# Kernel optimization log

Measured on AMD Instinct MI355X. Metric: run time of the kernel, lower is better.

## Reference

```python
import jax, jax.numpy as jnp
import numpy as np


def _conv1x1(x, w, b):
    # x: [B, Cin, T, H, W], w: [Cout, Cin], b: [Cout] -> [B, Cout, T, H, W]
    return jnp.einsum('bcthw,oc->bothw', x, w) + b[None, :, None, None, None]


def setup_inputs() -> dict:
    key = jax.random.key(0)
    ks = jax.random.split(key, 9)
    B, Ci, T, H, W = 2, 128, 4, 32, 32
    Co = 64
    s_in = 1.0 / np.sqrt(Ci)
    s_out = 1.0 / np.sqrt(Co)
    return {
        'z': jax.random.normal(ks[0], (B, Ci, T, H, W), dtype=jnp.float32),
        'w_theta': jax.random.uniform(ks[1], (Co, Ci), jnp.float32, -s_in, s_in),
        'b_theta': jax.random.uniform(ks[2], (Co,), jnp.float32, -s_in, s_in),
        'w_phi': jax.random.uniform(ks[3], (Co, Ci), jnp.float32, -s_in, s_in),
        'b_phi': jax.random.uniform(ks[4], (Co,), jnp.float32, -s_in, s_in),
        'w_psi': jax.random.uniform(ks[5], (Co, Ci), jnp.float32, -s_in, s_in),
        'b_psi': jax.random.uniform(ks[6], (Co,), jnp.float32, -s_in, s_in),
        'w_v': jax.random.uniform(ks[7], (Ci, Co), jnp.float32, -s_out, s_out),
        'b_v': jax.random.uniform(ks[8], (Ci,), jnp.float32, -s_out, s_out),
    }


def reference(z, w_theta, b_theta, w_phi, b_phi, w_psi, b_psi, w_v, b_v):
    B, Ci, T, H, W = z.shape
    Co = w_theta.shape[0]
    N = T * H * W
    # 1x1 conv projections, flattened to [B, Co, N]
    theta = _conv1x1(z, w_theta, b_theta).reshape(B, Co, N)
    phi = _conv1x1(z, w_phi, b_phi).reshape(B, Co, N)
    psi = _conv1x1(z, w_psi, b_psi).reshape(B, Co, N)
    # g = phi^T @ psi : [B, N, N]; normalize with ReLU(g / N)
    g = jnp.einsum('bcn,bcm->bnm', phi, psi)
    norm_g = jax.nn.relu(g / jnp.asarray(N, z.dtype))
    # tmp = norm_g @ theta^T -> [B, N, Co] -> [B, Co, T, H, W]
    tmp = jnp.einsum('bnm,bcm->bcn', norm_g, theta).reshape(B, Co, T, H, W)
    vg = _conv1x1(tmp, w_v, b_v)
    return vg + z
```

## Files before the change

kernel.cpp:

```cpp
#include <hip/hip_runtime.h>


#define NSEQ 4096
#define CI 128
#define CO 64

typedef __attribute__((ext_vector_type(8))) short bf16x8;
typedef __attribute__((ext_vector_type(4))) short bf16x4;
typedef __attribute__((ext_vector_type(4))) float f32x4;
typedef __attribute__((ext_vector_type(16))) float f32x16;

static __device__ inline short f2bf(float f) {
  union { float f; unsigned u; } v; v.f = f;
  unsigned r = v.u + 0x7fffu + ((v.u >> 16) & 1u);
  return (short)(r >> 16);
}
static __device__ inline float bf2f(short s) {
  union { unsigned u; float f; } v; v.u = ((unsigned)(unsigned short)s) << 16;
  return v.f;
}

#define MFMA1632(a, b, c) __builtin_amdgcn_mfma_f32_16x16x32_bf16(a, b, c, 0, 0, 0)
#define MFMA3216(a, b, c) __builtin_amdgcn_mfma_f32_32x32x16_bf16(a, b, c, 0, 0, 0)

#if __has_builtin(__builtin_amdgcn_mfma_f32_16x16x16bf16_1k)
static __device__ inline f32x4 mfma16(bf16x4 a, bf16x4 b, f32x4 c) {
  return __builtin_amdgcn_mfma_f32_16x16x16bf16_1k(a, b, c, 0, 0, 0);
}
#else
static __device__ inline f32x4 mfma16(bf16x4 a, bf16x4 b, f32x4 c) {
  asm("v_mfma_f32_16x16x16_bf16 %0, %1, %2, %0" : "+v"(c) : "v"(a), "v"(b));
  return c;
}
#endif

static __device__ inline unsigned cvt_pk_bf16(float lo, float hi) {
  unsigned d;
  asm("v_cvt_pk_bf16_f32 %0, %1, %2" : "=v"(d) : "v"(lo), "v"(hi));
  return d;
}
static __device__ inline void pl32swap(unsigned& a, unsigned& b) {
  asm("v_permlane32_swap_b32 %0, %1" : "+v"(a), "+v"(b));
}

__global__ __launch_bounds__(256, 2) void proj_kernel(
    const float* __restrict__ z,
    const float* __restrict__ w_th, const float* __restrict__ b_th,
    const float* __restrict__ w_ph, const float* __restrict__ b_ph,
    const float* __restrict__ w_ps, const float* __restrict__ b_ps,
    short* __restrict__ Qg, short* __restrict__ Kg, short* __restrict__ Vt)
{
  const int bid = blockIdx.x;
  const int b = bid >> 8;
  const int n0 = (bid & 255) * 16;
  const int t = threadIdx.x;
  const int w = t >> 6, l = t & 63, lr = l & 15, lg = l >> 4;
  const f32x4 zero4 = {0.f, 0.f, 0.f, 0.f};

  bf16x8 zf[4];
#pragma unroll
  for (int ks = 0; ks < 4; ++ks) {
    const float* zp = z + (size_t)(b * CI + ks * 32 + lg * 8) * NSEQ + n0 + lr;
    float tmp[8];
#pragma unroll
    for (int j = 0; j < 8; ++j) tmp[j] = zp[(size_t)j * NSEQ];
#pragma unroll
    for (int j = 0; j < 8; ++j) zf[ks][j] = f2bf(tmp[j]);
  }

  {
    const float* Wm[2] = {w_ph, w_ps};
    const float* Bm[2] = {b_ph, b_ps};
    short*       Dm[2] = {Qg, Kg};
#pragma unroll
    for (int mt = 0; mt < 2; ++mt) {
      const float sc = (mt == 0) ? (1.0f / 4096.0f) : 1.0f;
      f32x4 acc = zero4;
#pragma unroll
      for (int ks = 0; ks < 4; ++ks) {
        const float* wp = Wm[mt] + (size_t)(w * 16 + lr) * CI + ks * 32 + lg * 8;
        f32x4 x0 = *(const f32x4*)wp;
        f32x4 x1 = *(const f32x4*)(wp + 4);
        bf16x8 wf;
#pragma unroll
        for (int j = 0; j < 4; ++j) { wf[j] = f2bf(x0[j] * sc); wf[4 + j] = f2bf(x1[j] * sc); }
        acc = MFMA1632(wf, zf[ks], acc);
      }
      const f32x4 bias4 = *(const f32x4*)(Bm[mt] + w * 16 + lg * 4);
      bf16x4 pk;
#pragma unroll
      for (int r = 0; r < 4; ++r) pk[r] = f2bf(acc[r] + bias4[r] * sc);
      *(bf16x4*)(Dm[mt] + (size_t)(b * NSEQ + n0 + lr) * CO + w * 16 + lg * 4) = pk;
    }
  }

  {
    f32x4 acc = zero4;
#pragma unroll
    for (int ks = 0; ks < 4; ++ks) {
      const float* wp = w_th + (size_t)(w * 16 + lr) * CI + ks * 32 + lg * 8;
      f32x4 x0 = *(const f32x4*)wp;
      f32x4 x1 = *(const f32x4*)(wp + 4);
      bf16x8 wtf;
#pragma unroll
      for (int j = 0; j < 4; ++j) { wtf[j] = f2bf(x0[j]); wtf[4 + j] = f2bf(x1[j]); }
      acc = MFMA1632(zf[ks], wtf, acc);
    }
    const float bias = b_th[w * 16 + lr];
    bf16x4 pk;
#pragma unroll
    for (int r = 0; r < 4; ++r) pk[r] = f2bf(acc[r] + bias);
    *(bf16x4*)(Vt + (size_t)(b * CO + w * 16 + lr) * NSEQ + n0 + lg * 4) = pk;
  }
}

__global__ __launch_bounds__(256, 4) void attn_kernel(
    const short* __restrict__ Qg, const short* __restrict__ Kg,
    const short* __restrict__ Vt, short* __restrict__ Opart)
{
  __shared__ float red[2][2048];

  const int bid = blockIdx.x;
  const int ms = bid & 7;
  const int u = bid >> 3;
  const int b = u & 1;
  const int nt = u >> 1;
  const int n0 = nt * 32;
  const int t = threadIdx.x;
  const int w = t >> 6, l = t & 63, lc = l & 31, h = l >> 5;
  const int mw = ms * 512 + w * 128;

  bf16x8 qf[4];
  {
    const short* qb = Qg + (size_t)(b * NSEQ + n0 + lc) * CO + h * 8;
#pragma unroll
    for (int ks = 0; ks < 4; ++ks) qf[ks] = *(const bf16x8*)(qb + ks * 16);
  }

  f32x16 oacc[2];
#pragma unroll
  for (int i = 0; i < 2; ++i)
#pragma unroll
    for (int e = 0; e < 16; ++e) oacc[i][e] = 0.f;

#pragma unroll
  for (int it = 0; it < 4; ++it) {
    const int m0 = mw + it * 32;

    bf16x8 kf[4];
    {
      const short* kb = Kg + (size_t)(b * NSEQ + m0 + lc) * CO + h * 8;
#pragma unroll
      for (int ks = 0; ks < 4; ++ks) kf[ks] = *(const bf16x8*)(kb + ks * 16);
    }

    f32x16 s;
#pragma unroll
    for (int e = 0; e < 16; ++e) s[e] = 0.f;
#pragma unroll
    for (int ks = 0; ks < 4; ++ks) s = MFMA3216(kf[ks], qf[ks], s);

    unsigned pk[8];
#pragma unroll
    for (int q = 0; q < 8; ++q)
      pk[q] = cvt_pk_bf16(fmaxf(s[2 * q], 0.f), fmaxf(s[2 * q + 1], 0.f));

    const short* vb = Vt + (size_t)(b * CO + lc) * NSEQ + m0 + h * 8;
#pragma unroll
    for (int kw = 0; kw < 2; ++kw) {
      unsigned x0 = pk[4 * kw + 0], y0 = pk[4 * kw + 2];
      unsigned x1 = pk[4 * kw + 1], y1 = pk[4 * kw + 3];
      pl32swap(x0, y0); pl32swap(x1, y1);
      union { unsigned u[4]; bf16x8 v; } pb = {{x0, x1, y0, y1}};
      bf16x8 vf0 = *(const bf16x8*)(vb + kw * 16);
      bf16x8 vf1 = *(const bf16x8*)(vb + (size_t)32 * NSEQ + kw * 16);
      oacc[0] = MFMA3216(vf0, pb.v, oacc[0]);
      oacc[1] = MFMA3216(vf1, pb.v, oacc[1]);
    }
  }

  if (!(w & 1)) {
#pragma unroll
    for (int osub = 0; osub < 2; ++osub)
#pragma unroll
      for (int rb = 0; rb < 4; ++rb) {
        f32x4 v;
#pragma unroll
        for (int r = 0; r < 4; ++r) v[r] = oacc[osub][rb * 4 + r];
        const int o = osub * 32 + rb * 8 + h * 4;
        const int os = o ^ ((lc & 15) << 2);
        *(f32x4*)&red[w >> 1][lc * 64 + os] = v;
      }
  }
  __syncthreads();
  if (w & 1) {
#pragma unroll
    for (int osub = 0; osub < 2; ++osub)
#pragma unroll
      for (int rb = 0; rb < 4; ++rb) {
        const int o = osub * 32 + rb * 8 + h * 4;
        const int os = o ^ ((lc & 15) << 2);
        float* p = &red[w >> 1][lc * 64 + os];
        f32x4 v = *(f32x4*)p;
#pragma unroll
        for (int r = 0; r < 4; ++r) v[r] += oacc[osub][rb * 4 + r];
        *(f32x4*)p = v;
      }
  }
  __syncthreads();

  short* gout = Opart + (size_t)((b * 128 + nt) * 8 + ms) * 2048;
#pragma unroll
  for (int pass = 0; pass < 2; ++pass) {
    const int lin = pass * 1024 + t * 4;
    const int n = lin >> 6, os4 = lin & 63;
    f32x4 v0 = *(f32x4*)&red[0][lin];
    f32x4 v1 = *(f32x4*)&red[1][lin];
    const int o = os4 ^ ((n & 15) << 2);
    bf16x4 pkv;
#pragma unroll
    for (int r = 0; r < 4; ++r) pkv[r] = f2bf(v0[r] + v1[r]);
    *(bf16x4*)(gout + n * 64 + o) = pkv;
  }
}

__global__ __launch_bounds__(256, 2) void epi_kernel(
    const short* __restrict__ Opart, const float* __restrict__ w_v,
    const float* __restrict__ b_v, const float* __restrict__ z,
    float* __restrict__ out)
{
  __shared__ float Olds[16 * 68];

  const int bid = blockIdx.x;
  const int b = bid >> 8;
  const int n16 = bid & 255;
  const int nt = n16 >> 1, sub = n16 & 1;
  const int n0 = n16 * 16;
  const int t = threadIdx.x;

  {
    const short* src = Opart + (size_t)((b * 128 + nt) * 8) * 2048 + sub * 1024;
    const int n = t >> 4, o4 = (t & 15) * 4;
    f32x4 acc = {0.f, 0.f, 0.f, 0.f};
#pragma unroll
    for (int p = 0; p < 8; ++p) {
      bf16x4 vv = *(const bf16x4*)(src + (size_t)p * 2048 + n * 64 + o4);
#pragma unroll
      for (int j = 0; j < 4; ++j) acc[j] += bf2f(vv[j]);
    }
    *(f32x4*)&Olds[n * 68 + o4] = acc;
  }
  __syncthreads();

  const int w = t >> 6, l = t & 63, lr = l & 15, lg = l >> 4;
  const f32x4 zero4 = {0.f, 0.f, 0.f, 0.f};

  bf16x4 of[4];
#pragma unroll
  for (int osub = 0; osub < 4; ++osub)
#pragma unroll
    for (int j = 0; j < 4; ++j)
      of[osub][j] = f2bf(Olds[lr * 68 + osub * 16 + lg * 4 + j]);

#pragma unroll
  for (int c2 = 0; c2 < 2; ++c2) {
    const int cis = w * 2 + c2;
    bf16x4 wfr[4];
#pragma unroll
    for (int osub = 0; osub < 4; ++osub) {
      f32x4 wl = *(const f32x4*)(w_v + (size_t)(cis * 16 + lr) * CO + osub * 16 + lg * 4);
#pragma unroll
      for (int j = 0; j < 4; ++j) wfr[osub][j] = f2bf(wl[j]);
    }
    const f32x4 bv4 = *(const f32x4*)(b_v + cis * 16 + lg * 4);
    f32x4 e = zero4;
#pragma unroll
    for (int osub = 0; osub < 4; ++osub)
      e = mfma16(wfr[osub], of[osub], e);
#pragma unroll
    for (int r = 0; r < 4; ++r) {
      const int ci = cis * 16 + lg * 4 + r;
      const size_t off = (size_t)(b * CI + ci) * NSEQ + n0 + lr;
      out[off] = e[r] + z[off] + bv4[r];
    }
  }
}

extern "C" void kernel_launch(void* const* d_in, const int* in_sizes, int n_in,
                              void* d_out, int out_size, void* d_ws, size_t ws_size,
                              hipStream_t stream) {
  const float* z    = (const float*)d_in[0];
  const float* w_th = (const float*)d_in[1];
  const float* b_th = (const float*)d_in[2];
  const float* w_ph = (const float*)d_in[3];
  const float* b_ph = (const float*)d_in[4];
  const float* w_ps = (const float*)d_in[5];
  const float* b_ps = (const float*)d_in[6];
  const float* w_v  = (const float*)d_in[7];
  const float* b_v  = (const float*)d_in[8];
  float* out = (float*)d_out;

  short* Qg = (short*)d_ws;
  short* Kg = Qg + 2 * NSEQ * CO;
  short* Vt = Kg + 2 * NSEQ * CO;
  short* Opart = Vt + 2 * NSEQ * CO;

  proj_kernel<<<512, 256, 0, stream>>>(z, w_th, b_th, w_ph, b_ph, w_ps, b_ps,
                                       Qg, Kg, Vt);
  attn_kernel<<<2048, 256, 0, stream>>>(Qg, Kg, Vt, Opart);
  epi_kernel<<<512, 256, 0, stream>>>(Opart, w_v, b_v, z, out);
}
```

Measured before the change: 121.3 us.

## Repartition attention blocks so each wave owns distinct query rows, drop intra-block reduction

Each attention block previously handled 32 query rows, with its 4 waves splitting the key range; the partial outputs were then reduced through LDS across waves. Now each wave owns its own 32 query rows within a 128-row tile and scans 256 keys, and the grid is halved to 1024 blocks with a 16-way key split. The cross-wave LDS reduction and a sync go away, and partials are written transposed as [o][n] with 16-byte stores. In exchange the epilogue must sum 16 partials instead of 8, so Opart traffic roughly doubles, and the key loop is no longer unrolled.

After: 129.2 us. 1.06x slower.

```diff
diff --git a/kernel.cpp b/kernel.cpp
--- a/kernel.cpp
+++ b/kernel.cpp
@@ -118,21 +118,19 @@
     const short* __restrict__ Qg, const short* __restrict__ Kg,
     const short* __restrict__ Vt, short* __restrict__ Opart)
 {
-  __shared__ float red[2][2048];
+  __shared__ float lds_t[64 * 128];
 
   const int bid = blockIdx.x;
-  const int ms = bid & 7;
-  const int u = bid >> 3;
-  const int b = u & 1;
-  const int nt = u >> 1;
-  const int n0 = nt * 32;
+  const int s = (bid & 7) + ((bid >> 8) << 3);
+  const int nt = (bid >> 3) & 31;
+  const int b = s & 1, ms = s >> 1;
   const int t = threadIdx.x;
   const int w = t >> 6, l = t & 63, lc = l & 31, h = l >> 5;
-  const int mw = ms * 512 + w * 128;
+  const int n0w = nt * 128 + w * 32;
 
   bf16x8 qf[4];
   {
-    const short* qb = Qg + (size_t)(b * NSEQ + n0 + lc) * CO + h * 8;
+    const short* qb = Qg + (size_t)(b * NSEQ + n0w + lc) * CO + h * 8;
 #pragma unroll
     for (int ks = 0; ks < 4; ++ks) qf[ks] = *(const bf16x8*)(qb + ks * 16);
   }
@@ -143,9 +141,8 @@
 #pragma unroll
     for (int e = 0; e < 16; ++e) oacc[i][e] = 0.f;
 
-#pragma unroll
-  for (int it = 0; it < 4; ++it) {
-    const int m0 = mw + it * 32;
+  for (int it = 0; it < 8; ++it) {
+    const int m0 = ms * 256 + it * 32;
 
     bf16x8 kf[4];
     {
@@ -154,16 +151,16 @@
       for (int ks = 0; ks < 4; ++ks) kf[ks] = *(const bf16x8*)(kb + ks * 16);
     }
 
-    f32x16 s;
-#pragma unroll
-    for (int e = 0; e < 16; ++e) s[e] = 0.f;
-#pragma unroll
-    for (int ks = 0; ks < 4; ++ks) s = MFMA3216(kf[ks], qf[ks], s);
+    f32x16 sx;
+#pragma unroll
+    for (int e = 0; e < 16; ++e) sx[e] = 0.f;
+#pragma unroll
+    for (int ks = 0; ks < 4; ++ks) sx = MFMA3216(kf[ks], qf[ks], sx);
 
     unsigned pk[8];
 #pragma unroll
     for (int q = 0; q < 8; ++q)
-      pk[q] = cvt_pk_bf16(fmaxf(s[2 * q], 0.f), fmaxf(s[2 * q + 1], 0.f));
+      pk[q] = cvt_pk_bf16(fmaxf(sx[2 * q], 0.f), fmaxf(sx[2 * q + 1], 0.f));
 
     const short* vb = Vt + (size_t)(b * CO + lc) * NSEQ + m0 + h * 8;
 #pragma unroll
@@ -179,48 +176,29 @@
     }
   }
 
-  if (!(w & 1)) {
-#pragma unroll
-    for (int osub = 0; osub < 2; ++osub)
-#pragma unroll
-      for (int rb = 0; rb < 4; ++rb) {
-        f32x4 v;
-#pragma unroll
-        for (int r = 0; r < 4; ++r) v[r] = oacc[osub][rb * 4 + r];
-        const int o = osub * 32 + rb * 8 + h * 4;
-        const int os = o ^ ((lc & 15) << 2);
-        *(f32x4*)&red[w >> 1][lc * 64 + os] = v;
+#pragma unroll
+  for (int osub = 0; osub < 2; ++osub)
+#pragma unroll
+    for (int rb = 0; rb < 4; ++rb)
+#pragma unroll
+      for (int r = 0; r < 4; ++r) {
+        const int o = osub * 32 + rb * 8 + h * 4 + r;
+        lds_t[o * 128 + w * 32 + lc] = oacc[osub][rb * 4 + r];
       }
-  }
   __syncthreads();
-  if (w & 1) {
-#pragma unroll
-    for (int osub = 0; osub < 2; ++osub)
-#pragma unroll
-      for (int rb = 0; rb < 4; ++rb) {
-        const int o = osub * 32 + rb * 8 + h * 4;
-        const int os = o ^ ((lc & 15) << 2);
-        float* p = &red[w >> 1][lc * 64 + os];
-        f32x4 v = *(f32x4*)p;
-#pragma unroll
-        for (int r = 0; r < 4; ++r) v[r] += oacc[osub][rb * 4 + r];
-        *(f32x4*)p = v;
-      }
-  }
-  __syncthreads();
-
-  short* gout = Opart + (size_t)((b * 128 + nt) * 8 + ms) * 2048;
-#pragma unroll
-  for (int pass = 0; pass < 2; ++pass) {
-    const int lin = pass * 1024 + t * 4;
-    const int n = lin >> 6, os4 = lin & 63;
-    f32x4 v0 = *(f32x4*)&red[0][lin];
-    f32x4 v1 = *(f32x4*)&red[1][lin];
-    const int o = os4 ^ ((n & 15) << 2);
-    bf16x4 pkv;
-#pragma unroll
-    for (int r = 0; r < 4; ++r) pkv[r] = f2bf(v0[r] + v1[r]);
-    *(bf16x4*)(gout + n * 64 + o) = pkv;
+
+  short* gout = Opart + (size_t)((b * 32 + nt) * 16 + ms) * 8192;
+  {
+    const int o = t >> 2, nq = (t & 3) * 32;
+    const float* src = lds_t + o * 128 + nq;
+    unsigned outw[16];
+#pragma unroll
+    for (int q = 0; q < 16; ++q) outw[q] = cvt_pk_bf16(src[2 * q], src[2 * q + 1]);
+#pragma unroll
+    for (int c4 = 0; c4 < 4; ++c4) {
+      union { unsigned u[4]; bf16x8 v; } pkv = {{outw[4*c4], outw[4*c4+1], outw[4*c4+2], outw[4*c4+3]}};
+      *(bf16x8*)(gout + o * 128 + nq + c4 * 8) = pkv.v;
+    }
   }
 }
 
@@ -234,21 +212,22 @@
   const int bid = blockIdx.x;
   const int b = bid >> 8;
   const int n16 = bid & 255;
-  const int nt = n16 >> 1, sub = n16 & 1;
+  const int nt = n16 >> 3, sub = n16 & 7;
   const int n0 = n16 * 16;
   const int t = threadIdx.x;
 
   {
-    const short* src = Opart + (size_t)((b * 128 + nt) * 8) * 2048 + sub * 1024;
-    const int n = t >> 4, o4 = (t & 15) * 4;
+    const short* src = Opart + (size_t)((b * 32 + nt) * 16) * 8192 + sub * 16;
+    const int o = t >> 2, n4 = (t & 3) * 4;
     f32x4 acc = {0.f, 0.f, 0.f, 0.f};
 #pragma unroll
-    for (int p = 0; p < 8; ++p) {
-      bf16x4 vv = *(const bf16x4*)(src + (size_t)p * 2048 + n * 64 + o4);
+    for (int p = 0; p < 16; ++p) {
+      bf16x4 vv = *(const bf16x4*)(src + (size_t)p * 8192 + o * 128 + n4);
 #pragma unroll
       for (int j = 0; j < 4; ++j) acc[j] += bf2f(vv[j]);
     }
-    *(f32x4*)&Olds[n * 68 + o4] = acc;
+#pragma unroll
+    for (int j = 0; j < 4; ++j) Olds[(n4 + j) * 68 + o] = acc[j];
   }
   __syncthreads();
 
@@ -307,6 +286,6 @@
 
   proj_kernel<<<512, 256, 0, stream>>>(z, w_th, b_th, w_ph, b_ph, w_ps, b_ps,
                                        Qg, Kg, Vt);
-  attn_kernel<<<2048, 256, 0, stream>>>(Qg, Kg, Vt, Opart);
+  attn_kernel<<<1024, 256, 0, stream>>>(Qg, Kg, Vt, Opart);
   epi_kernel<<<512, 256, 0, stream>>>(Opart, w_v, b_v, z, out);
 }
```
